# Performance work log

Measured on AMD Instinct MI355X. Metric: run time of the kernel, lower is better.

## Reference

```python
import jax, jax.numpy as jnp
import numpy as np

G, K = 4, 3
P = K * K  # n_offset_points


def _conv(x, w, b, groups=1):
    # x: [B,C,H,W] NCHW, w: [O, I/groups, kh, kw] (torch OIHW), padding=1 -> SAME
    y = jax.lax.conv_general_dilated(x, w, (1, 1), 'SAME', feature_group_count=groups)
    return y + b[None, :, None, None]


def setup_inputs() -> dict:
    key = jax.random.key(0)
    ks = jax.random.split(key, 9)
    B, C, H, W = 4, 256, 64, 64
    Cg = C // G
    s = 0.05
    return {
        'x': jax.random.normal(ks[0], (B, H * W, C), jnp.float32),
        'off_w1': jax.random.normal(ks[1], (C, Cg, 3, 3), jnp.float32) * s,
        'off_b1': jax.random.normal(ks[2], (C,), jnp.float32) * s,
        'off_w2': jax.random.normal(ks[3], (G * 2 * P, C, 3, 3), jnp.float32) * s,
        'off_b2': jax.random.normal(ks[4], (G * 2 * P,), jnp.float32) * s,
        'mod_w1': jax.random.normal(ks[5], (C // 4, C, 3, 3), jnp.float32) * s,
        'mod_b1': jax.random.normal(ks[6], (C // 4,), jnp.float32) * s,
        'mod_w2': jax.random.normal(ks[7], (G * P, C // 4, 3, 3), jnp.float32) * s,
        'mod_b2': jax.random.normal(ks[8], (G * P,), jnp.float32) * s,
        'H': 64,
        'W': 64,
    }


def reference(x, off_w1, off_b1, off_w2, off_b2, mod_w1, mod_b1, mod_w2, mod_b2, H, W):
    B, N, C = x.shape
    Cg = C // G
    x2d = x.transpose(0, 2, 1).reshape(B, C, H, W)

    # offset branch (grouped 3x3 conv -> GELU -> 3x3 conv), offset_scale = 1.0
    h = jax.nn.gelu(_conv(x2d, off_w1, off_b1, groups=G), approximate=False)
    off = _conv(h, off_w2, off_b2).reshape(B, G, 2, P, H, W)
    # modulation branch
    m = jax.nn.gelu(_conv(x2d, mod_w1, mod_b1), approximate=False)
    mod = jax.nn.sigmoid(_conv(m, mod_w2, mod_b2)).reshape(B, G, P, H, W)

    # base kernel offsets: base[0]=x, base[1]=y, each [P]
    rv = jnp.arange(-(K - 1) // 2, (K - 1) // 2 + 1, dtype=x.dtype)
    by, bx = jnp.meshgrid(rv, rv, indexing='ij')
    bx, by = bx.reshape(P), by.reshape(P)

    yg, xg = jnp.meshgrid(jnp.arange(H, dtype=x.dtype), jnp.arange(W, dtype=x.dtype), indexing='ij')
    # sampling coords in pixel space; clamp to [-1,1] normalized (align_corners=True)
    # is exactly clamp to [0, W-1] / [0, H-1] in pixel space, and border padding
    # then never goes out of range.
    px = jnp.clip(xg + bx[:, None, None] + off[:, :, 0], 0.0, W - 1)  # [B,G,P,H,W]
    py = jnp.clip(yg + by[:, None, None] + off[:, :, 1], 0.0, H - 1)

    x0f, y0f = jnp.floor(px), jnp.floor(py)
    wx, wy = px - x0f, py - y0f
    x0 = x0f.astype(jnp.int32)
    y0 = y0f.astype(jnp.int32)
    x1 = jnp.minimum(x0 + 1, W - 1)
    y1 = jnp.minimum(y0 + 1, H - 1)

    flat = x2d.reshape(B, G, Cg, H * W)

    def gather(yi, xi):
        idx = (yi * W + xi).reshape(B, G, 1, P, H * W)
        return jnp.take_along_axis(flat[:, :, :, None, :], idx, axis=-1)  # [B,G,Cg,P,HW]

    wxr = wx.reshape(B, G, 1, P, H * W)
    wyr = wy.reshape(B, G, 1, P, H * W)
    v = (gather(y0, x0) * (1 - wxr) * (1 - wyr)
         + gather(y0, x1) * wxr * (1 - wyr)
         + gather(y1, x0) * (1 - wxr) * wyr
         + gather(y1, x1) * wxr * wyr)
    v = v * mod.reshape(B, G, 1, P, H * W)
    out = v.mean(axis=3)  # average over offset points -> [B,G,Cg,HW]
    return out.reshape(B, C, H * W).transpose(0, 2, 1)
```

## Files before the change

### kernel.cpp

```cpp
#include <hip/hip_runtime.h>
#include <math.h>


#define SLAB 4369
#define AGAP 1056

typedef __attribute__((ext_vector_type(8))) short short8;
typedef __attribute__((ext_vector_type(4))) float floatx4;

__device__ __forceinline__ unsigned short f2bf(float f) {
    unsigned u = __float_as_uint(f);
    u = (u + 0x7FFFu + ((u >> 16) & 1u)) >> 16;
    return (unsigned short)u;
}
__device__ __forceinline__ float bf2f(unsigned short h) {
    return __uint_as_float(((unsigned)h) << 16);
}
__device__ __forceinline__ void split2(float v, unsigned short* hi, unsigned short* lo) {
    unsigned short h = f2bf(v);
    *hi = h;
    *lo = f2bf(v - bf2f(h));
}
__device__ __forceinline__ float gelu_exact(float v) {
    return 0.5f * v * (1.0f + erff(v * 0.70710678118654752f));
}

template<int NC, int NTAPS, int MT, int NT, int ACT, int OUTMODE>
__device__ __forceinline__ void conv_core(
    const unsigned short* __restrict__ ah, const unsigned short* __restrict__ al,
    int aC0,
    const unsigned short* __restrict__ wh, const unsigned short* __restrict__ wl,
    const float* __restrict__ bias,
    int b, int mblock, int tap0,
    unsigned short* __restrict__ oh, unsigned short* __restrict__ ol,
    int oC0,
    float* __restrict__ pf)
{
    const int OCPAD = NT * 16;
    const int TOTAL = NTAPS * NC;
    int wave = threadIdx.x >> 6;
    int lane = threadIdx.x & 63;
    int quad = lane >> 4;
    int l16 = lane & 15;

    int pix0 = (mblock * 4 + wave) * (MT * 16);
    int y = pix0 >> 6;
    int x0 = pix0 & 63;

    floatx4 acc[MT][NT];
#pragma unroll
    for (int nt = 0; nt < NT; nt++) {
        float bv = (OUTMODE == 1) ? bias[nt * 16 + l16] : 0.f;
#pragma unroll
        for (int mt = 0; mt < MT; mt++) { floatx4 v = {bv, bv, bv, bv}; acc[mt][nt] = v; }
    }

    short8 A0h[MT], A0l[MT], B0h[NT], B0l[NT];
    short8 A1h[MT], A1l[MT], B1h[NT], B1l[NT];

#define LOAD_FRAG(AH_, AL_, BH_, BL_, IT_) do {                                       \
    const int ch_  = (IT_) / NTAPS;                                                   \
    const int tap_ = tap0 + (IT_) % NTAPS;                                            \
    const int kh_ = tap_ / 3, kw_ = tap_ - kh_ * 3;                                   \
    size_t r_ = ((size_t)((aC0 + ch_) * 4 + b) * SLAB                                 \
                 + (y + kh_) * 66 + (x0 + kw_) + l16) * 32 + quad * 8;                \
    _Pragma("unroll")                                                                 \
    for (int mt = 0; mt < MT; mt++) {                                                 \
        AH_[mt] = *(const short8*)(ah + r_ + (size_t)(mt * 16) * 32);                 \
        AL_[mt] = *(const short8*)(al + r_ + (size_t)(mt * 16) * 32);                 \
    }                                                                                 \
    size_t wr_ = ((size_t)(ch_ * 9 + tap_) * OCPAD + l16) * 32 + quad * 8;            \
    _Pragma("unroll")                                                                 \
    for (int nt = 0; nt < NT; nt++) {                                                 \
        BH_[nt] = *(const short8*)(wh + wr_ + (size_t)(nt * 16) * 32);                \
        BL_[nt] = *(const short8*)(wl + wr_ + (size_t)(nt * 16) * 32);                \
    }                                                                                 \
    __builtin_amdgcn_sched_barrier(0);                                                \
} while (0)

#define DO_MFMA(AH_, AL_, BH_, BL_) do {                                              \
    _Pragma("unroll")                                                                 \
    for (int nt = 0; nt < NT; nt++) {                                                 \
        _Pragma("unroll")                                                             \
        for (int mt = 0; mt < MT; mt++) {                                             \
            acc[mt][nt] = __builtin_amdgcn_mfma_f32_16x16x32_bf16(AH_[mt], BH_[nt], acc[mt][nt], 0, 0, 0); \
            acc[mt][nt] = __builtin_amdgcn_mfma_f32_16x16x32_bf16(AH_[mt], BL_[nt], acc[mt][nt], 0, 0, 0); \
            acc[mt][nt] = __builtin_amdgcn_mfma_f32_16x16x32_bf16(AL_[mt], BH_[nt], acc[mt][nt], 0, 0, 0); \
        }                                                                             \
    }                                                                                 \
} while (0)

    LOAD_FRAG(A0h, A0l, B0h, B0l, 0);
#pragma unroll 1
    for (int it = 0; it < TOTAL - 2; it += 2) {
        LOAD_FRAG(A1h, A1l, B1h, B1l, it + 1);
        DO_MFMA(A0h, A0l, B0h, B0l);
        LOAD_FRAG(A0h, A0l, B0h, B0l, it + 2);
        DO_MFMA(A1h, A1l, B1h, B1l);
    }
    LOAD_FRAG(A1h, A1l, B1h, B1l, TOTAL - 1);
    DO_MFMA(A0h, A0l, B0h, B0l);
    DO_MFMA(A1h, A1l, B1h, B1l);

#undef LOAD_FRAG
#undef DO_MFMA

#pragma unroll
    for (int nt = 0; nt < NT; nt++) {
        int oc = nt * 16 + l16;
#pragma unroll
        for (int mt = 0; mt < MT; mt++) {
#pragma unroll
            for (int r = 0; r < 4; r++) {
                float v = acc[mt][nt][r];
                int px = pix0 + mt * 16 + quad * 4 + r;
                if (OUTMODE == 2) {
                    atomicAdd(pf + ((size_t)b * 4096 + px) * OCPAD + oc, v);
                } else if (OUTMODE == 3) {
                    pf[((size_t)b * 4096 + px) * OCPAD + oc] = v;
                } else {
                    if (ACT == 1) v = gelu_exact(v);
                    else if (ACT == 2) v = 1.0f / (1.0f + expf(-v));
                    int yy = (px >> 6) + 1, xx = (px & 63) + 1;
                    int och = oC0 + (oc >> 5);
                    size_t o = ((size_t)(och * 4 + b) * SLAB + yy * 66 + xx) * 32 + (oc & 31);
                    unsigned short hv, lv; split2(v, &hv, &lv);
                    oh[o] = hv; ol[o] = lv;
                }
            }
        }
    }
}

__global__ __launch_bounds__(256, 1) void convA_kernel(
    const unsigned short* __restrict__ xph, const unsigned short* __restrict__ xpl,
    const unsigned short* __restrict__ w1h, const unsigned short* __restrict__ w1l,
    const float* __restrict__ off_b1,
    const unsigned short* __restrict__ w3h, const unsigned short* __restrict__ w3l,
    unsigned short* __restrict__ h1h, unsigned short* __restrict__ h1l,
    float* __restrict__ P3)
{
    int bx = blockIdx.x;
    int xcd = bx & 7;
    int j = bx >> 3;
    int pair = xcd * 8 + j / 7;
    int role = j % 7;
    int mb = pair & 15;
    int b = pair >> 4;
    if (role < 4) {
        int g = role;
        conv_core<2, 9, 4, 4, 1, 1>(xph, xpl, g * 2,
            w1h + (size_t)g * 2 * 9 * 64 * 32, w1l + (size_t)g * 2 * 9 * 64 * 32,
            off_b1 + g * 64,
            b, mb, 0, h1h, h1l, g * 2, nullptr);
    } else {
        int ks = role - 4;
        conv_core<8, 3, 4, 4, 0, 2>(xph, xpl, 0, w3h, w3l, nullptr,
            b, mb, ks * 3, nullptr, nullptr, 0, P3);
    }
}

__global__ __launch_bounds__(256) void finalizeA_kernel(
    const float* __restrict__ P3, const float* __restrict__ mod_b1,
    unsigned short* __restrict__ m1h, unsigned short* __restrict__ m1l)
{
    int idx = blockIdx.x * 256 + threadIdx.x;
    int c = idx & 63;
    int p = idx >> 6;
    int b = p >> 12;
    int px = p & 4095;
    int rem = ((px >> 6) + 1) * 66 + (px & 63) + 1;
    float u = P3[(size_t)p * 64 + c] + mod_b1[c];
    u = gelu_exact(u);
    size_t o = ((size_t)((c >> 5) * 4 + b) * SLAB + rem) * 32 + (c & 31);
    unsigned short hu, lu; split2(u, &hu, &lu);
    m1h[o] = hu; m1l[o] = lu;
}

__global__ __launch_bounds__(256, 1) void convB_kernel(
    const unsigned short* __restrict__ h1h, const unsigned short* __restrict__ h1l,
    const unsigned short* __restrict__ w2h, const unsigned short* __restrict__ w2l,
    const unsigned short* __restrict__ m1h, const unsigned short* __restrict__ m1l,
    const unsigned short* __restrict__ w4h, const unsigned short* __restrict__ w4l,
    float* __restrict__ P2a, float* __restrict__ P4a)
{
    int bx = blockIdx.x;
    if (bx < 192) {
        int xcd = bx & 7;
        int j = bx >> 3;
        int pair = xcd * 8 + j / 3;
        int ks = j % 3;
        int mb = pair & 15;
        int b = pair >> 4;
        conv_core<8, 3, 4, 5, 0, 2>(h1h, h1l, 0, w2h, w2l, nullptr,
            b, mb, ks * 3, nullptr, nullptr, 0, P2a);
    } else {
        int t = bx - 192;
        int xcd = t & 7;
        int q = t >> 3;
        int pair = xcd * 8 + q;
        int mb = pair & 15;
        int b = pair >> 4;
        conv_core<2, 9, 4, 3, 0, 3>(m1h, m1l, 0, w4h, w4l, nullptr,
            b, mb, 0, nullptr, nullptr, 0, P4a);
    }
}

#define ZBLK 2304
#define RBLK 1040
#define XBLK 17424
#define WBLK 1980
__global__ void prep_all_kernel(
    const float* __restrict__ x,
    const float* __restrict__ w1f, const float* __restrict__ w2f,
    const float* __restrict__ w3f, const float* __restrict__ w4f,
    unsigned short* __restrict__ xph, unsigned short* __restrict__ xpl,
    unsigned short* __restrict__ h1h, unsigned short* __restrict__ h1l,
    unsigned short* __restrict__ m1h, unsigned short* __restrict__ m1l,
    unsigned short* __restrict__ w1h, unsigned short* __restrict__ w1l,
    unsigned short* __restrict__ w2h, unsigned short* __restrict__ w2l,
    unsigned short* __restrict__ w3h, unsigned short* __restrict__ w3l,
    unsigned short* __restrict__ w4h, unsigned short* __restrict__ w4l,
    float* __restrict__ accf)
{
    int blk = blockIdx.x;
    int t = threadIdx.x;
    if (blk < ZBLK) {
        ((uint4*)accf)[(size_t)blk * 256 + t] = make_uint4(0u, 0u, 0u, 0u);
        return;
    }
    blk -= ZBLK;
    if (blk < RBLK) {
        int b = blk / 260;
        int r = blk - b * 260;
        int i, j;
        if (r < 66)       { i = 0;        j = r; }
        else if (r < 132) { i = 65;       j = r - 66; }
        else if (r < 196) { i = r - 131;  j = 0; }
        else              { i = r - 195;  j = 65; }
        size_t pp = (size_t)i * 66 + j;
        int ch = t >> 5, sub = t & 31;
        size_t o = ((size_t)(ch * 4 + b) * SLAB + pp) * 32 + sub;
        h1h[o] = 0; h1l[o] = 0;
        if (t < 64) { m1h[o] = 0; m1l[o] = 0; }
        return;
    }
    blk -= RBLK;
    if (blk < XBLK) {
        int b = blk / 4356;
        int rem = blk - b * 4356;
        int i = rem / 66, j = rem - i * 66;
        float v = 0.f;
        if (i >= 1 && i <= 64 && j >= 1 && j <= 64)
            v = x[((size_t)b * 4096 + (size_t)(i - 1) * 64 + (j - 1)) * 256 + t];
        size_t o = ((size_t)((t >> 5) * 4 + b) * SLAB + rem) * 32 + (t & 31);
        unsigned short h, l; split2(v, &h, &l);
        xph[o] = h; xpl[o] = l;
        return;
    }
    blk -= XBLK;
    {
        const int N1 = 147456, N2 = 184320, N3 = 147456, N4 = 27648;
        int idx = blk * 256 + t;
        const float* w; unsigned short *outh, *outl;
        int ocpad, oc_real, ic, base;
        if (idx < N1)                { w = w1f; outh = w1h; outl = w1l; ocpad = 64; oc_real = 64; ic = 64;  base = 0; }
        else if (idx < N1 + N2)      { w = w2f; outh = w2h; outl = w2l; ocpad = 80; oc_real = 72; ic = 256; base = N1; }
        else if (idx < N1 + N2 + N3) { w = w3f; outh = w3h; outl = w3l; ocpad = 64; oc_real = 64; ic = 256; base = N1 + N2; }
        else                         { w = w4f; outh = w4h; outl = w4l; ocpad = 48; oc_real = 36; ic = 64;  base = N1 + N2 + N3; }
        int lidx = idx - base;
        int ici = lidx & 31;
        int t1 = lidx >> 5;
        int ocp = t1 % ocpad;
        int t2 = t1 / ocpad;
        int tap = t2 % 9;
        int t3 = t2 / 9;
        int nch = ic >> 5;
        int ch = t3 % nch;
        int g = t3 / nch;
        float v = 0.f;
        if (ocp < oc_real) {
            int oc = g * oc_real + ocp;
            int icx = ch * 32 + ici;
            v = w[((size_t)oc * ic + icx) * 9 + tap];
        }
        unsigned short h, l; split2(v, &h, &l);
        outh[lidx] = h; outl[lidx] = l;
    }
}

__global__ __launch_bounds__(256) void deform_sample(
    const float* __restrict__ x,
    const float* __restrict__ P2a, const float* __restrict__ P4a,
    const float* __restrict__ b2, const float* __restrict__ b4,
    float* __restrict__ out)
{
    int bid = (int)((blockIdx.x & 7u) * 512u + (blockIdx.x >> 3));
    int wid = (int)(((unsigned)bid * 256u + threadIdx.x) >> 6);
    int lane = (int)(threadIdx.x & 63u);
    int sub = lane >> 4;
    int li = lane & 15;

    int b = wid >> 12;
    int rem = wid & 4095;
    int g = rem >> 10;
    int hw = ((rem & 1023) << 2) + sub;
    int hy = hw >> 6;
    int wx = hw & 63;

    float fx = 0.f, fy = 0.f, fm = 0.f;
    if (li < 9) {
        size_t p = (size_t)(b << 12) + hw;
        int c2 = g * 18 + li;
        fx = P2a[p * 80 + c2] + b2[c2];
        fy = P2a[p * 80 + 9 + c2] + b2[9 + c2];
        int c4 = g * 9 + li;
        float mv = P4a[p * 48 + c4] + b4[c4];
        fm = 1.0f / (1.0f + expf(-mv));
    }
    float px = fminf(fmaxf((float)wx + (float)(li % 3 - 1) + fx, 0.f), 63.f);
    float py = fminf(fmaxf((float)hy + (float)(li / 3 - 1) + fy, 0.f), 63.f);
    float x0f = floorf(px), y0f = floorf(py);
    float wxf = px - x0f, wyf = py - y0f;
    int x0 = (int)x0f, y0 = (int)y0f;
    int x1 = min(x0 + 1, 63), y1 = min(y0 + 1, 63);

    const float4* xb = (const float4*)(x + ((size_t)(b << 12)) * 256 + g * 64 + li * 4);
    float4 acc = make_float4(0.f, 0.f, 0.f, 0.f);
    int sb = sub << 4;
#pragma unroll
    for (int q = 0; q < 9; q++) {
        int src = sb + q;
        int   qx0 = __shfl(x0, src);
        int   qx1 = __shfl(x1, src);
        int   qy0 = __shfl(y0, src);
        int   qy1 = __shfl(y1, src);
        float qwx = __shfl(wxf, src);
        float qwy = __shfl(wyf, src);
        float qm  = __shfl(fm, src);
        float4 v00 = xb[(size_t)(qy0 * 64 + qx0) * 64];
        float4 v01 = xb[(size_t)(qy0 * 64 + qx1) * 64];
        float4 v10 = xb[(size_t)(qy1 * 64 + qx0) * 64];
        float4 v11 = xb[(size_t)(qy1 * 64 + qx1) * 64];
        float w00 = (1.f - qwx) * (1.f - qwy);
        float w01 = qwx * (1.f - qwy);
        float w10 = (1.f - qwx) * qwy;
        float w11 = qwx * qwy;
        acc.x += qm * (v00.x * w00 + v01.x * w01 + v10.x * w10 + v11.x * w11);
        acc.y += qm * (v00.y * w00 + v01.y * w01 + v10.y * w10 + v11.y * w11);
        acc.z += qm * (v00.z * w00 + v01.z * w01 + v10.z * w10 + v11.z * w11);
        acc.w += qm * (v00.w * w00 + v01.w * w01 + v10.w * w10 + v11.w * w11);
    }
    const float s = 1.f / 9.f;
    acc.x *= s; acc.y *= s; acc.z *= s; acc.w *= s;
    float4* ob = (float4*)(out + ((size_t)(b << 12) + hw) * 256 + g * 64 + li * 4);
    *ob = acc;
}

extern "C" void kernel_launch(void* const* d_in, const int* in_sizes, int n_in,
                              void* d_out, int out_size, void* d_ws, size_t ws_size,
                              hipStream_t stream)
{
    const float* x      = (const float*)d_in[0];
    const float* off_w1 = (const float*)d_in[1];
    const float* off_b1 = (const float*)d_in[2];
    const float* off_w2 = (const float*)d_in[3];
    const float* off_b2 = (const float*)d_in[4];
    const float* mod_w1 = (const float*)d_in[5];
    const float* mod_b1 = (const float*)d_in[6];
    const float* mod_w2 = (const float*)d_in[7];
    const float* mod_b2 = (const float*)d_in[8];

    const size_t XP = 8u * 4u * SLAB * 32u;
    const size_t MP = 2u * 4u * SLAB * 32u;
    const size_t W1 = 4u * 2u * 9u * 64u * 32u;
    const size_t W2 = 8u * 9u * 80u * 32u;
    const size_t W3 = 8u * 9u * 64u * 32u;
    const size_t W4 = 2u * 9u * 48u * 32u;

    unsigned short* ws = (unsigned short*)d_ws;
    size_t o = 0;
    unsigned short* xph = ws + o; o += XP + AGAP;
    unsigned short* xpl = ws + o; o += XP + AGAP;
    unsigned short* h1h = ws + o; o += XP + AGAP;
    unsigned short* h1l = ws + o; o += XP + AGAP;
    unsigned short* m1h = ws + o; o += MP + AGAP;
    unsigned short* m1l = ws + o; o += MP + AGAP;
    unsigned short* w1h = ws + o; o += W1 + AGAP;
    unsigned short* w1l = ws + o; o += W1 + AGAP;
    unsigned short* w2h = ws + o; o += W2 + AGAP;
    unsigned short* w2l = ws + o; o += W2 + AGAP;
    unsigned short* w3h = ws + o; o += W3 + AGAP;
    unsigned short* w3l = ws + o; o += W3 + AGAP;
    unsigned short* w4h = ws + o; o += W4 + AGAP;
    unsigned short* w4l = ws + o; o += W4 + AGAP;
    o += o & 1;
    float* fbase = (float*)(ws + o);
    float* P3  = fbase;
    float* P2a = P3 + (size_t)4 * 4096 * 64;
    float* P4a = P2a + (size_t)4 * 4096 * 80;
    const size_t ACC_FLOATS = (size_t)4 * 4096 * (64 + 80 + 48);
    size_t need_bytes = o * 2 + ACC_FLOATS * 4;
    if (ws_size < need_bytes) return;

    prep_all_kernel<<<ZBLK + RBLK + XBLK + WBLK, 256, 0, stream>>>(
        x, off_w1, off_w2, mod_w1, mod_w2,
        xph, xpl, h1h, h1l, m1h, m1l,
        w1h, w1l, w2h, w2l, w3h, w3l, w4h, w4l, P3);

    convA_kernel<<<dim3(448, 1, 1), 256, 0, stream>>>(xph, xpl, w1h, w1l, off_b1,
                                                      w3h, w3l, h1h, h1l, P3);
    finalizeA_kernel<<<4096, 256, 0, stream>>>(P3, mod_b1, m1h, m1l);
    convB_kernel<<<dim3(256, 1, 1), 256, 0, stream>>>(h1h, h1l, w2h, w2l,
                                                      m1h, m1l, w4h, w4l, P2a, P4a);
    deform_sample<<<4096, 256, 0, stream>>>(x, P2a, P4a, off_b2, mod_b2, (float*)d_out);
}
```

Before: 209.1 us.

## Stage conv input halo tiles and weights through LDS for shared tap reuse

```diff
diff --git a/kernel.cpp b/kernel.cpp
--- a/kernel.cpp
+++ b/kernel.cpp
@@ -4,6 +4,9 @@
 
 #define SLAB 4369
 #define AGAP 1056
+#define APXS 40
+#define AROW (66*APXS)
+#define AHALF (6*AROW)
 
 typedef __attribute__((ext_vector_type(8))) short short8;
 typedef __attribute__((ext_vector_type(4))) float floatx4;
@@ -25,8 +28,9 @@
     return 0.5f * v * (1.0f + erff(v * 0.70710678118654752f));
 }
 
-template<int NC, int NTAPS, int MT, int NT, int ACT, int OUTMODE>
-__device__ __forceinline__ void conv_core(
+template<int NC, int NTAPS, int NT, int ACT, int OUTMODE>
+__device__ __forceinline__ void conv_core_lds(
+    unsigned short* lds,
     const unsigned short* __restrict__ ah, const unsigned short* __restrict__ al,
     int aC0,
     const unsigned short* __restrict__ wh, const unsigned short* __restrict__ wl,
@@ -37,79 +41,96 @@
     float* __restrict__ pf)
 {
     const int OCPAD = NT * 16;
-    const int TOTAL = NTAPS * NC;
-    int wave = threadIdx.x >> 6;
-    int lane = threadIdx.x & 63;
+    unsigned short* Ahl = lds;
+    unsigned short* All = lds + AHALF;
+    unsigned short* Bhl = lds + 2 * AHALF;
+    unsigned short* Bll = lds + 2 * AHALF + OCPAD * APXS;
+
+    int tid = (int)threadIdx.x;
+    int wave = tid >> 6;
+    int lane = tid & 63;
     int quad = lane >> 4;
     int l16 = lane & 15;
 
-    int pix0 = (mblock * 4 + wave) * (MT * 16);
-    int y = pix0 >> 6;
-    int x0 = pix0 & 63;
-
-    floatx4 acc[MT][NT];
+    int pix0 = (mblock * 4 + wave) * 64;
+    int y0 = mblock * 4;
+
+    floatx4 acc[4][NT];
 #pragma unroll
     for (int nt = 0; nt < NT; nt++) {
         float bv = (OUTMODE == 1) ? bias[nt * 16 + l16] : 0.f;
 #pragma unroll
-        for (int mt = 0; mt < MT; mt++) { floatx4 v = {bv, bv, bv, bv}; acc[mt][nt] = v; }
-    }
-
-    short8 A0h[MT], A0l[MT], B0h[NT], B0l[NT];
-    short8 A1h[MT], A1l[MT], B1h[NT], B1l[NT];
-
-#define LOAD_FRAG(AH_, AL_, BH_, BL_, IT_) do {                                       \
-    const int ch_  = (IT_) / NTAPS;                                                   \
-    const int tap_ = tap0 + (IT_) % NTAPS;                                            \
-    const int kh_ = tap_ / 3, kw_ = tap_ - kh_ * 3;                                   \
-    size_t r_ = ((size_t)((aC0 + ch_) * 4 + b) * SLAB                                 \
-                 + (y + kh_) * 66 + (x0 + kw_) + l16) * 32 + quad * 8;                \
-    _Pragma("unroll")                                                                 \
-    for (int mt = 0; mt < MT; mt++) {                                                 \
-        AH_[mt] = *(const short8*)(ah + r_ + (size_t)(mt * 16) * 32);                 \
-        AL_[mt] = *(const short8*)(al + r_ + (size_t)(mt * 16) * 32);                 \
-    }                                                                                 \
-    size_t wr_ = ((size_t)(ch_ * 9 + tap_) * OCPAD + l16) * 32 + quad * 8;            \
-    _Pragma("unroll")                                                                 \
-    for (int nt = 0; nt < NT; nt++) {                                                 \
-        BH_[nt] = *(const short8*)(wh + wr_ + (size_t)(nt * 16) * 32);                \
-        BL_[nt] = *(const short8*)(wl + wr_ + (size_t)(nt * 16) * 32);                \
-    }                                                                                 \
-    __builtin_amdgcn_sched_barrier(0);                                                \
-} while (0)
-
-#define DO_MFMA(AH_, AL_, BH_, BL_) do {                                              \
-    _Pragma("unroll")                                                                 \
-    for (int nt = 0; nt < NT; nt++) {                                                 \
-        _Pragma("unroll")                                                             \
-        for (int mt = 0; mt < MT; mt++) {                                             \
-            acc[mt][nt] = __builtin_amdgcn_mfma_f32_16x16x32_bf16(AH_[mt], BH_[nt], acc[mt][nt], 0, 0, 0); \
-            acc[mt][nt] = __builtin_amdgcn_mfma_f32_16x16x32_bf16(AH_[mt], BL_[nt], acc[mt][nt], 0, 0, 0); \
-            acc[mt][nt] = __builtin_amdgcn_mfma_f32_16x16x32_bf16(AL_[mt], BH_[nt], acc[mt][nt], 0, 0, 0); \
-        }                                                                             \
-    }                                                                                 \
-} while (0)
-
-    LOAD_FRAG(A0h, A0l, B0h, B0l, 0);
+        for (int mt = 0; mt < 4; mt++) { floatx4 v = {bv, bv, bv, bv}; acc[mt][nt] = v; }
+    }
+
 #pragma unroll 1
-    for (int it = 0; it < TOTAL - 2; it += 2) {
-        LOAD_FRAG(A1h, A1l, B1h, B1l, it + 1);
-        DO_MFMA(A0h, A0l, B0h, B0l);
-        LOAD_FRAG(A0h, A0l, B0h, B0l, it + 2);
-        DO_MFMA(A1h, A1l, B1h, B1l);
-    }
-    LOAD_FRAG(A1h, A1l, B1h, B1l, TOTAL - 1);
-    DO_MFMA(A0h, A0l, B0h, B0l);
-    DO_MFMA(A1h, A1l, B1h, B1l);
-
-#undef LOAD_FRAG
-#undef DO_MFMA
+    for (int ch = 0; ch < NC; ch++) {
+        {
+            size_t gbase = ((size_t)((aC0 + ch) * 4 + b) * SLAB + (size_t)y0 * 66) * 32;
+#pragma unroll
+            for (int k = 0; k < 7; k++) {
+                int u = k * 256 + tid;
+                if (u < 1584) {
+                    int px = u >> 2, j = u & 3;
+                    int row = px / 66, col = px - row * 66;
+                    int dst = row * AROW + col * APXS + j * 8;
+                    *(short8*)(Ahl + dst) = *(const short8*)(ah + gbase + (size_t)u * 8);
+                    *(short8*)(All + dst) = *(const short8*)(al + gbase + (size_t)u * 8);
+                }
+            }
+        }
+#pragma unroll 1
+        for (int tp = 0; tp < NTAPS; tp++) {
+            int tap = tap0 + tp;
+            int kh = tap / 3, kw = tap - kh * 3;
+            {
+                size_t wbase = (size_t)(ch * 9 + tap) * OCPAD * 32;
+                const int BU = OCPAD * 4;
+#pragma unroll
+                for (int k = 0; k * 256 < BU; k++) {
+                    int u = k * 256 + tid;
+                    if (u < BU) {
+                        int oc = u >> 2, j = u & 3;
+                        int dst = oc * APXS + j * 8;
+                        *(short8*)(Bhl + dst) = *(const short8*)(wh + wbase + (size_t)u * 8);
+                        *(short8*)(Bll + dst) = *(const short8*)(wl + wbase + (size_t)u * 8);
+                    }
+                }
+            }
+            __syncthreads();
+
+            short8 Afh[4], Afl[4], Bfh[NT], Bfl[NT];
+            int arow = (wave + kh) * AROW;
+#pragma unroll
+            for (int mt = 0; mt < 4; mt++) {
+                int aoff = arow + (kw + l16 + mt * 16) * APXS + quad * 8;
+                Afh[mt] = *(const short8*)(Ahl + aoff);
+                Afl[mt] = *(const short8*)(All + aoff);
+            }
+#pragma unroll
+            for (int nt = 0; nt < NT; nt++) {
+                int boff = (nt * 16 + l16) * APXS + quad * 8;
+                Bfh[nt] = *(const short8*)(Bhl + boff);
+                Bfl[nt] = *(const short8*)(Bll + boff);
+            }
+#pragma unroll
+            for (int nt = 0; nt < NT; nt++) {
+#pragma unroll
+                for (int mt = 0; mt < 4; mt++) {
+                    acc[mt][nt] = __builtin_amdgcn_mfma_f32_16x16x32_bf16(Afh[mt], Bfh[nt], acc[mt][nt], 0, 0, 0);
+                    acc[mt][nt] = __builtin_amdgcn_mfma_f32_16x16x32_bf16(Afh[mt], Bfl[nt], acc[mt][nt], 0, 0, 0);
+                    acc[mt][nt] = __builtin_amdgcn_mfma_f32_16x16x32_bf16(Afl[mt], Bfh[nt], acc[mt][nt], 0, 0, 0);
+                }
+            }
+            __syncthreads();
+        }
+    }
 
 #pragma unroll
     for (int nt = 0; nt < NT; nt++) {
         int oc = nt * 16 + l16;
 #pragma unroll
-        for (int mt = 0; mt < MT; mt++) {
+        for (int mt = 0; mt < 4; mt++) {
 #pragma unroll
             for (int r = 0; r < 4; r++) {
                 float v = acc[mt][nt][r];
@@ -140,6 +161,7 @@
     unsigned short* __restrict__ h1h, unsigned short* __restrict__ h1l,
     float* __restrict__ P3)
 {
+    __shared__ unsigned short lds[2 * AHALF + 2 * 64 * APXS];
     int bx = blockIdx.x;
     int xcd = bx & 7;
     int j = bx >> 3;
@@ -149,13 +171,13 @@
     int b = pair >> 4;
     if (role < 4) {
         int g = role;
-        conv_core<2, 9, 4, 4, 1, 1>(xph, xpl, g * 2,
+        conv_core_lds<2, 9, 4, 1, 1>(lds, xph, xpl, g * 2,
             w1h + (size_t)g * 2 * 9 * 64 * 32, w1l + (size_t)g * 2 * 9 * 64 * 32,
             off_b1 + g * 64,
             b, mb, 0, h1h, h1l, g * 2, nullptr);
     } else {
         int ks = role - 4;
-        conv_core<8, 3, 4, 4, 0, 2>(xph, xpl, 0, w3h, w3l, nullptr,
+        conv_core_lds<8, 3, 4, 0, 2>(lds, xph, xpl, 0, w3h, w3l, nullptr,
             b, mb, ks * 3, nullptr, nullptr, 0, P3);
     }
 }
@@ -184,6 +206,7 @@
     const unsigned short* __restrict__ w4h, const unsigned short* __restrict__ w4l,
     float* __restrict__ P2a, float* __restrict__ P4a)
 {
+    __shared__ unsigned short lds[2 * AHALF + 2 * 80 * APXS];
     int bx = blockIdx.x;
     if (bx < 192) {
         int xcd = bx & 7;
@@ -192,7 +215,7 @@
         int ks = j % 3;
         int mb = pair & 15;
         int b = pair >> 4;
-        conv_core<8, 3, 4, 5, 0, 2>(h1h, h1l, 0, w2h, w2l, nullptr,
+        conv_core_lds<8, 3, 5, 0, 2>(lds, h1h, h1l, 0, w2h, w2l, nullptr,
             b, mb, ks * 3, nullptr, nullptr, 0, P2a);
     } else {
         int t = bx - 192;
@@ -201,7 +224,7 @@
         int pair = xcd * 8 + q;
         int mb = pair & 15;
         int b = pair >> 4;
-        conv_core<2, 9, 4, 3, 0, 3>(m1h, m1l, 0, w4h, w4l, nullptr,
+        conv_core_lds<2, 9, 3, 0, 3>(lds, m1h, m1l, 0, w4h, w4l, nullptr,
             b, mb, 0, nullptr, nullptr, 0, P4a);
     }
 }
```

New measurement: 216.6 us. +3.6%, slower.
